# Kernel tuning notes

Measured on AMD Instinct MI355X. Metric: run time of the kernel, lower is better.

Reference implementation:

```python
import jax, jax.numpy as jnp
import numpy as np

N = 100000
E = 1600000
F_IN = 128
HID = 64
HEADS = 2
OUT_HEADS = 1
NUM_CLASS = 18
NEG_SLOPE = 0.2


def setup_inputs() -> dict:
    key = jax.random.key(0)
    ks = jax.random.split(key, 12)
    x = jax.random.normal(ks[0], (N, F_IN), dtype=jnp.float32)
    edge_index = jax.random.randint(ks[1], (2, E), 0, N, dtype=jnp.int64)
    s = lambda k, shp, fan: jax.random.normal(k, shp, dtype=jnp.float32) * (1.0 / np.sqrt(fan))
    W0 = s(ks[2], (F_IN, HID), F_IN)
    b0 = jnp.zeros((HID,), dtype=jnp.float32)
    W1 = s(ks[3], (HID, HEADS * HID), HID)
    att_src1 = s(ks[4], (HEADS, HID), HID)
    att_dst1 = s(ks[5], (HEADS, HID), HID)
    b1 = jnp.zeros((HEADS * HID,), dtype=jnp.float32)
    W2 = s(ks[6], (HEADS * HID, OUT_HEADS * NUM_CLASS), HEADS * HID)
    att_src2 = s(ks[7], (OUT_HEADS, NUM_CLASS), NUM_CLASS)
    att_dst2 = s(ks[8], (OUT_HEADS, NUM_CLASS), NUM_CLASS)
    b2 = jnp.zeros((OUT_HEADS * NUM_CLASS,), dtype=jnp.float32)
    return {"x": x, "edge_index": edge_index, "W0": W0, "b0": b0,
            "W1": W1, "att_src1": att_src1, "att_dst1": att_dst1, "b1": b1,
            "W2": W2, "att_src2": att_src2, "att_dst2": att_dst2, "b2": b2}


def gat_conv(x, src, dst, W, att_s, att_d, bias, heads, out_ch):
    n = x.shape[0]
    h = (x @ W).reshape(n, heads, out_ch)              # [N,H,C]
    a_s = jnp.sum(h * att_s, axis=-1)                   # [N,H]
    a_d = jnp.sum(h * att_d, axis=-1)                   # [N,H]
    e = jax.nn.leaky_relu(a_s[src] + a_d[dst], NEG_SLOPE)  # [E,H]
    m = jax.ops.segment_max(e, dst, num_segments=n)
    ex = jnp.exp(e - m[dst])
    denom = jax.ops.segment_sum(ex, dst, num_segments=n)
    alpha = ex / denom[dst]                              # [E,H]
    msg = h[src] * alpha[:, :, None]                     # [E,H,C]
    out = jax.ops.segment_sum(msg, dst, num_segments=n)  # [N,H,C]
    return out.reshape(n, heads * out_ch) + bias


def reference(x, edge_index, W0, b0, W1, att_src1, att_dst1, b1, W2, att_src2, att_dst2, b2):
    n = x.shape[0]
    # PyG GATConv adds self-loops by default
    loops = jnp.arange(n, dtype=edge_index.dtype)
    src = jnp.concatenate([edge_index[0], loops])
    dst = jnp.concatenate([edge_index[1], loops])
    # eval mode: dropout is identity
    h = jax.nn.relu(x @ W0 + b0)
    h = jax.nn.elu(gat_conv(h, src, dst, W1, att_src1, att_dst1, b1, HEADS, HID))
    out = gat_conv(h, src, dst, W2, att_src2, att_dst2, b2, OUT_HEADS, NUM_CLASS)
    return jax.nn.log_softmax(out, axis=-1)
```

## Files before the change

### kernel.cpp

```cpp
#include <hip/hip_runtime.h>
#include <math.h>


#define NEG_SLOPE 0.2f
#define STASH_CAP 128

typedef unsigned short ushort_t;

__device__ __forceinline__ float wmax(float v) {
    for (int o = 32; o; o >>= 1) v = fmaxf(v, __shfl_xor(v, o));
    return v;
}
__device__ __forceinline__ float wsum(float v) {
    for (int o = 32; o; o >>= 1) v += __shfl_xor(v, o);
    return v;
}

__device__ __forceinline__ unsigned bfpack(float a, float b) {
    unsigned ua = __float_as_uint(a);
    unsigned ub = __float_as_uint(b);
    ua = (ua + 0x7fffu + ((ua >> 16) & 1u)) >> 16;
    ub = (ub + 0x7fffu + ((ub >> 16) & 1u)) & 0xffff0000u;
    return ua | ub;
}
__device__ __forceinline__ ushort_t bf16of(float a) {
    unsigned ua = __float_as_uint(a);
    return (ushort_t)((ua + 0x7fffu + ((ua >> 16) & 1u)) >> 16);
}
__device__ __forceinline__ float bflo(unsigned u) { return __uint_as_float(u << 16); }
__device__ __forceinline__ float bfhi(unsigned u) { return __uint_as_float(u & 0xffff0000u); }
__device__ __forceinline__ float bfval(ushort_t u) { return __uint_as_float(((unsigned)u) << 16); }

__global__ void k_deg_init(int* __restrict__ deg, int N) {
    int i = blockIdx.x * blockDim.x + threadIdx.x;
    if (i < N) deg[i] = 1;
}
__global__ void k_deg_edges(const int* __restrict__ ei, int* __restrict__ deg,
                            int* __restrict__ eofs, int E) {
    int e = blockIdx.x * blockDim.x + threadIdx.x;
    if (e < E) eofs[e] = atomicAdd(&deg[ei[E + e]], 1);
}

__global__ __launch_bounds__(256) void k_scan1(const int* __restrict__ deg, int* __restrict__ rs,
                                               int* __restrict__ bsum, int N) {
    __shared__ int s[256];
    int t = threadIdx.x;
    int base = blockIdx.x * 1024;
    int i0 = base + t * 4;
    int d0 = (i0 + 0 < N) ? deg[i0 + 0] : 0;
    int d1 = (i0 + 1 < N) ? deg[i0 + 1] : 0;
    int d2 = (i0 + 2 < N) ? deg[i0 + 2] : 0;
    int d3 = (i0 + 3 < N) ? deg[i0 + 3] : 0;
    int s0 = d0, s1 = s0 + d1, s2 = s1 + d2, s3 = s2 + d3;
    int tsum = s3;
    s[t] = tsum;
    __syncthreads();
    for (int off = 1; off < 256; off <<= 1) {
        int v = (t >= off) ? s[t - off] : 0;
        __syncthreads();
        s[t] += v;
        __syncthreads();
    }
    int excl = s[t] - tsum;
    if (i0 + 0 < N) rs[1 + i0 + 0] = excl + s0;
    if (i0 + 1 < N) rs[1 + i0 + 1] = excl + s1;
    if (i0 + 2 < N) rs[1 + i0 + 2] = excl + s2;
    if (i0 + 3 < N) rs[1 + i0 + 3] = excl + s3;
    if (t == 0) bsum[blockIdx.x] = s[255];
}

__global__ __launch_bounds__(256) void k_scan2(const int* __restrict__ bsum,
                                               int* __restrict__ boff, int NB) {
    __shared__ int s[256];
    int t = threadIdx.x;
    int orig = (t < NB) ? bsum[t] : 0;
    s[t] = orig;
    __syncthreads();
    for (int off = 1; off < 256; off <<= 1) {
        int v = (t >= off) ? s[t - off] : 0;
        __syncthreads();
        s[t] += v;
        __syncthreads();
    }
    if (t < NB) boff[t] = s[t] - orig;
}

__global__ void k_scan3(int* __restrict__ rs, const int* __restrict__ boff, int N) {
    int i = blockIdx.x * blockDim.x + threadIdx.x;
    if (i == 0) rs[0] = 0;
    if (i < N) rs[1 + i] += boff[i >> 10];
}

__global__ __launch_bounds__(256) void k_scatter(const int* __restrict__ ei,
                                                 const int* __restrict__ eofs,
                                                 const int* __restrict__ rs,
                                                 int* __restrict__ csr,
                                                 int E, int Etot, int cohortBlocks) {
    int c = blockIdx.x & 7;
    int pb = blockIdx.x >> 3;
    int tid = pb * 256 + threadIdx.x;
    int stride = cohortBlocks * 256;
    for (int e = tid; e < Etot; e += stride) {
        int dst = (e < E) ? ei[E + e] : (e - E);
        if (((dst >> 13) & 7) != c) continue;
        int src, ofs;
        if (e < E) { src = ei[e]; ofs = eofs[e]; } else { src = dst; ofs = 0; }
        csr[rs[dst] + ofs] = src;
    }
}


__global__ __launch_bounds__(256) void k_gemm1(const float* __restrict__ x,
                                               const float* __restrict__ W0,
                                               const float* __restrict__ b0,
                                               unsigned* __restrict__ h0b, int N) {
    __shared__ float wl[128 * 64];
    __shared__ float al[64 * 132];
    int t = threadIdx.x;
    int n0 = blockIdx.x * 64;
    const float4* wg = (const float4*)W0;
    float4* wl4 = (float4*)wl;
#pragma unroll
    for (int i = 0; i < 8; ++i) wl4[t + i * 256] = wg[t + i * 256];
#pragma unroll
    for (int i = 0; i < 8; ++i) {
        int f = t + i * 256;
        int node = f >> 5, q = f & 31;
        int ng = n0 + node; if (ng > N - 1) ng = N - 1;
        float4 v = ((const float4*)x)[(size_t)ng * 32 + q];
        *(float4*)&al[node * 132 + q * 4] = v;
    }
    __syncthreads();
    int colg = t & 15;
    int rowg = t >> 4;
    float4 acc[4];
#pragma unroll
    for (int j = 0; j < 4; ++j) acc[j] = make_float4(0.f, 0.f, 0.f, 0.f);
    for (int k4 = 0; k4 < 128; k4 += 4) {
        float4 w0 = *(float4*)&wl[(k4 + 0) * 64 + colg * 4];
        float4 w1 = *(float4*)&wl[(k4 + 1) * 64 + colg * 4];
        float4 w2 = *(float4*)&wl[(k4 + 2) * 64 + colg * 4];
        float4 w3 = *(float4*)&wl[(k4 + 3) * 64 + colg * 4];
#pragma unroll
        for (int j = 0; j < 4; ++j) {
            float4 a = *(float4*)&al[(rowg * 4 + j) * 132 + k4];
            acc[j].x += a.x * w0.x + a.y * w1.x + a.z * w2.x + a.w * w3.x;
            acc[j].y += a.x * w0.y + a.y * w1.y + a.z * w2.y + a.w * w3.y;
            acc[j].z += a.x * w0.z + a.y * w1.z + a.z * w2.z + a.w * w3.z;
            acc[j].w += a.x * w0.w + a.y * w1.w + a.z * w2.w + a.w * w3.w;
        }
    }
    float4 bb = ((const float4*)b0)[colg];
#pragma unroll
    for (int j = 0; j < 4; ++j) {
        int n = n0 + rowg * 4 + j;
        if (n < N) {
            float rx = fmaxf(acc[j].x + bb.x, 0.f);
            float ry = fmaxf(acc[j].y + bb.y, 0.f);
            float rz = fmaxf(acc[j].z + bb.z, 0.f);
            float rw = fmaxf(acc[j].w + bb.w, 0.f);
            uint2 pr; pr.x = bfpack(rx, ry); pr.y = bfpack(rz, rw);
            ((uint2*)h0b)[(size_t)n * 16 + colg] = pr;
        }
    }
}

__global__ __launch_bounds__(256) void k_gemm2(const unsigned* __restrict__ h0b,
                                               const float* __restrict__ W1,
                                               const float* __restrict__ as_g,
                                               const float* __restrict__ ad_g,
                                               ushort_t* __restrict__ h1b,
                                               float* __restrict__ as1,
                                               float* __restrict__ ad1, int N) {
    __shared__ float wl[64 * 128];
    __shared__ float al[64 * 68];
    int t = threadIdx.x;
    int n0 = blockIdx.x * 64;
    const float4* wg = (const float4*)W1;
    float4* wl4 = (float4*)wl;
#pragma unroll
    for (int i = 0; i < 8; ++i) wl4[t + i * 256] = wg[t + i * 256];
#pragma unroll
    for (int i = 0; i < 2; ++i) {
        int f = t + i * 256;
        int node = f >> 3, q = f & 7;
        int ng = n0 + node; if (ng > N - 1) ng = N - 1;
        uint4 u = ((const uint4*)h0b)[(size_t)ng * 8 + q];
        float* dst = &al[node * 68 + q * 8];
        dst[0] = bflo(u.x); dst[1] = bfhi(u.x);
        dst[2] = bflo(u.y); dst[3] = bfhi(u.y);
        dst[4] = bflo(u.z); dst[5] = bfhi(u.z);
        dst[6] = bflo(u.w); dst[7] = bfhi(u.w);
    }
    __syncthreads();
    int colg = t & 31;
    int rowg = t >> 5;
    float4 acc[8];
#pragma unroll
    for (int j = 0; j < 8; ++j) acc[j] = make_float4(0.f, 0.f, 0.f, 0.f);
    for (int k4 = 0; k4 < 64; k4 += 4) {
        float4 w0 = *(float4*)&wl[(k4 + 0) * 128 + colg * 4];
        float4 w1 = *(float4*)&wl[(k4 + 1) * 128 + colg * 4];
        float4 w2 = *(float4*)&wl[(k4 + 2) * 128 + colg * 4];
        float4 w3 = *(float4*)&wl[(k4 + 3) * 128 + colg * 4];
#pragma unroll
        for (int j = 0; j < 8; ++j) {
            float4 a = *(float4*)&al[(rowg * 8 + j) * 68 + k4];
            acc[j].x += a.x * w0.x + a.y * w1.x + a.z * w2.x + a.w * w3.x;
            acc[j].y += a.x * w0.y + a.y * w1.y + a.z * w2.y + a.w * w3.y;
            acc[j].z += a.x * w0.z + a.y * w1.z + a.z * w2.z + a.w * w3.z;
            acc[j].w += a.x * w0.w + a.y * w1.w + a.z * w2.w + a.w * w3.w;
        }
    }
    float4 asv = ((const float4*)as_g)[colg];
    float4 adv = ((const float4*)ad_g)[colg];
    float ps[8], pd[8];
#pragma unroll
    for (int j = 0; j < 8; ++j) {
        ps[j] = acc[j].x * asv.x + acc[j].y * asv.y + acc[j].z * asv.z + acc[j].w * asv.w;
        pd[j] = acc[j].x * adv.x + acc[j].y * adv.y + acc[j].z * adv.z + acc[j].w * adv.w;
    }
    for (int o = 1; o < 16; o <<= 1) {
#pragma unroll
        for (int j = 0; j < 8; ++j) {
            ps[j] += __shfl_xor(ps[j], o);
            pd[j] += __shfl_xor(pd[j], o);
        }
    }
#pragma unroll
    for (int j = 0; j < 8; ++j) {
        int n = n0 + rowg * 8 + j;
        if (n < N) {
            uint2 pr;
            pr.x = bfpack(acc[j].x, acc[j].y);
            pr.y = bfpack(acc[j].z, acc[j].w);
            ((uint2*)h1b)[(size_t)n * 32 + colg] = pr;
        }
    }
    int lane = t & 63;
    if ((lane & 15) == 0) {
        int head = (lane >> 4) & 1;
#pragma unroll
        for (int j = 0; j < 8; ++j) {
            int n = n0 + rowg * 8 + j;
            if (n < N) {
                as1[n * 2 + head] = ps[j];
                ad1[n * 2 + head] = pd[j];
            }
        }
    }
}

__global__ __launch_bounds__(256) void k_node_l1(const int* __restrict__ rs,
                                                 const int* __restrict__ csr,
                                                 const ushort_t* __restrict__ h1b,
                                                 const float* __restrict__ as1,
                                                 const float* __restrict__ ad1,
                                                 const float* __restrict__ b1,
                                                 unsigned* __restrict__ aggb, int N) {
    __shared__ float2 stashA[4][128];
    __shared__ float4 stashE[4][STASH_CAP];
    int wid = threadIdx.x >> 6;
    int lane = threadIdx.x & 63;
    int n = (blockIdx.x * 256 + threadIdx.x) >> 6;
    if (n >= N) return;
    int row = rs[n], end = rs[n + 1];
    int deg = end - row;
    float2 adv = ((const float2*)ad1)[n];
    const float2* asp = (const float2*)as1;
    const char* h1base = (const char*)h1b;
    int eg = lane >> 4;
    int fl = lane & 15;
    int head_off = (fl >= 8) ? 64 : 0;
    int flbase = fl * 16;
    float acc[8] = {0.f, 0.f, 0.f, 0.f, 0.f, 0.f, 0.f, 0.f};
    float inv0, inv1;
    if (deg <= 64) {
        bool act = lane < deg;
        int src = act ? csr[row + lane] : 0;
        float2 av = asp[src];
        float e0 = av.x + adv.x, e1 = av.y + adv.y;
        e0 = e0 > 0.f ? e0 : NEG_SLOPE * e0;
        e1 = e1 > 0.f ? e1 : NEG_SLOPE * e1;
        if (!act) { e0 = -INFINITY; e1 = -INFINITY; }
        float m0 = wmax(e0), m1 = wmax(e1);
        float p0 = act ? __expf(e0 - m0) : 0.f;
        float p1 = act ? __expf(e1 - m1) : 0.f;
        inv0 = __builtin_amdgcn_rcpf(wsum(p0));
        inv1 = __builtin_amdgcn_rcpf(wsum(p1));
        stashA[wid][lane] = make_float2(__int_as_float(src), p0);
        stashA[wid][64 + lane] = make_float2(__int_as_float(src), p1);
        for (int j = 0; j < deg; j += 4) {
            float2 sa = stashA[wid][head_off + j + eg];
            int sj = __float_as_int(sa.x);
            float aj = sa.y;
            uint4 u = *(const uint4*)(h1base + (((unsigned)sj) << 8) + flbase);
            acc[0] += bflo(u.x) * aj; acc[1] += bfhi(u.x) * aj;
            acc[2] += bflo(u.y) * aj; acc[3] += bfhi(u.y) * aj;
            acc[4] += bflo(u.z) * aj; acc[5] += bfhi(u.z) * aj;
            acc[6] += bflo(u.w) * aj; acc[7] += bfhi(u.w) * aj;
        }
    } else {
        inv0 = 1.f; inv1 = 1.f;
        float m0 = -INFINITY, m1 = -INFINITY, l0 = 0.f, l1 = 0.f;
        for (int base = row; base < end; base += 64) {
            int idx = base + lane;
            bool act = idx < end;
            int src = act ? csr[idx] : 0;
            float2 av = asp[src];
            float e0 = av.x + adv.x, e1 = av.y + adv.y;
            e0 = e0 > 0.f ? e0 : NEG_SLOPE * e0;
            e1 = e1 > 0.f ? e1 : NEG_SLOPE * e1;
            int sidx = idx - row;
            if (act && sidx < STASH_CAP)
                stashE[wid][sidx] = make_float4(__int_as_float(src), e0, e1, 0.f);
            if (!act) { e0 = -INFINITY; e1 = -INFINITY; }
            float m0n = fmaxf(m0, wmax(e0));
            float m1n = fmaxf(m1, wmax(e1));
            float p0 = act ? __expf(e0 - m0n) : 0.f;
            float p1 = act ? __expf(e1 - m1n) : 0.f;
            l0 = l0 * __expf(m0 - m0n) + wsum(p0);
            l1 = l1 * __expf(m1 - m1n) + wsum(p1);
            m0 = m0n; m1 = m1n;
        }
        float r0 = __builtin_amdgcn_rcpf(l0);
        float r1 = __builtin_amdgcn_rcpf(l1);
        for (int base = row; base < end; base += 64) {
            int idx = base + lane;
            bool act = idx < end;
            int sidx = idx - row;
            int src; float e0, e1;
            if (sidx < STASH_CAP) {
                float4 se = stashE[wid][sidx];
                src = __float_as_int(se.x);
                e0 = se.y; e1 = se.z;
            } else {
                src = act ? csr[idx] : 0;
                float2 av = asp[src];
                e0 = av.x + adv.x; e1 = av.y + adv.y;
                e0 = e0 > 0.f ? e0 : NEG_SLOPE * e0;
                e1 = e1 > 0.f ? e1 : NEG_SLOPE * e1;
            }
            if (!act) src = 0;
            float a0 = act ? __expf(e0 - m0) * r0 : 0.f;
            float a1 = act ? __expf(e1 - m1) * r1 : 0.f;
            stashA[wid][lane] = make_float2(__int_as_float(src), a0);
            stashA[wid][64 + lane] = make_float2(__int_as_float(src), a1);
            int cnt = min(64, end - base);
            for (int j = 0; j < cnt; j += 4) {
                float2 sa = stashA[wid][head_off + j + eg];
                int sj = __float_as_int(sa.x);
                float aj = sa.y;
                uint4 u = *(const uint4*)(h1base + (((unsigned)sj) << 8) + flbase);
                acc[0] += bflo(u.x) * aj; acc[1] += bfhi(u.x) * aj;
                acc[2] += bflo(u.y) * aj; acc[3] += bfhi(u.y) * aj;
                acc[4] += bflo(u.z) * aj; acc[5] += bfhi(u.z) * aj;
                acc[6] += bflo(u.w) * aj; acc[7] += bfhi(u.w) * aj;
            }
        }
    }
#pragma unroll
    for (int i = 0; i < 8; ++i) {
        acc[i] += __shfl_xor(acc[i], 16);
        acc[i] += __shfl_xor(acc[i], 32);
    }
    if (lane < 16) {
        float inv = (lane >= 8) ? inv1 : inv0;
        float4 ba = ((const float4*)b1)[lane * 2];
        float4 bb4 = ((const float4*)b1)[lane * 2 + 1];
        float v[8];
        v[0] = acc[0] * inv + ba.x;  v[1] = acc[1] * inv + ba.y;
        v[2] = acc[2] * inv + ba.z;  v[3] = acc[3] * inv + ba.w;
        v[4] = acc[4] * inv + bb4.x; v[5] = acc[5] * inv + bb4.y;
        v[6] = acc[6] * inv + bb4.z; v[7] = acc[7] * inv + bb4.w;
#pragma unroll
        for (int i = 0; i < 8; ++i) v[i] = v[i] > 0.f ? v[i] : __expf(v[i]) - 1.f;
        uint4 pk;
        pk.x = bfpack(v[0], v[1]); pk.y = bfpack(v[2], v[3]);
        pk.z = bfpack(v[4], v[5]); pk.w = bfpack(v[6], v[7]);
        ((uint4*)aggb)[(size_t)n * 16 + lane] = pk;
    }
}

__global__ __launch_bounds__(256, 4) void k_node2(const unsigned* __restrict__ aggb,
                                                  const float* __restrict__ W2,
                                                  const float* __restrict__ as_g,
                                                  const float* __restrict__ ad_g,
                                                  ushort_t* __restrict__ h2b,
                                                  float* __restrict__ a_s,
                                                  float* __restrict__ a_d, int N) {
    __shared__ float al[64 * 132];
    __shared__ float w2t[20 * 132];
    int t = threadIdx.x;
    int n0 = blockIdx.x * 64;
#pragma unroll
    for (int i = 0; i < 4; ++i) {
        int f = t + i * 256;
        int node = f >> 4, q = f & 15;
        int ng = n0 + node; if (ng > N - 1) ng = N - 1;
        uint4 u = ((const uint4*)aggb)[(size_t)ng * 16 + q];
        float* dst = &al[node * 132 + q * 8];
        dst[0] = bflo(u.x); dst[1] = bfhi(u.x);
        dst[2] = bflo(u.y); dst[3] = bfhi(u.y);
        dst[4] = bflo(u.z); dst[5] = bfhi(u.z);
        dst[6] = bflo(u.w); dst[7] = bfhi(u.w);
    }
    for (int i = t; i < 2560; i += 256) {
        int c = i >> 7, k = i & 127;
        w2t[c * 132 + k] = (c < 18) ? W2[k * 18 + c] : 0.f;
    }
    __syncthreads();
    int node = t >> 2;
    int cq = t & 3;
    int c0 = cq * 5;
    int n = n0 + node;
    float acc[5] = {0.f, 0.f, 0.f, 0.f, 0.f};
#pragma unroll 2
    for (int k4 = 0; k4 < 128; k4 += 4) {
        float4 a = *(float4*)&al[node * 132 + k4];
#pragma unroll
        for (int i = 0; i < 5; ++i) {
            float4 w = *(float4*)&w2t[(c0 + i) * 132 + k4];
            acc[i] += a.x * w.x + a.y * w.y + a.z * w.z + a.w * w.w;
        }
    }
    float ps = 0.f, pd = 0.f;
#pragma unroll
    for (int i = 0; i < 5; ++i) {
        int c = c0 + i;
        float asv = (c < 18) ? as_g[c] : 0.f;
        float adv = (c < 18) ? ad_g[c] : 0.f;
        ps += acc[i] * asv;
        pd += acc[i] * adv;
    }
    ps += __shfl_xor(ps, 1); ps += __shfl_xor(ps, 2);
    pd += __shfl_xor(pd, 1); pd += __shfl_xor(pd, 2);
    if (n < N) {
#pragma unroll
        for (int i = 0; i < 5; ++i) {
            int c = c0 + i;
            if (c < 18) h2b[(size_t)n * 24 + c] = bf16of(acc[i]);
        }
        if (cq == 0) { a_s[n] = ps; a_d[n] = pd; }
    }
}

__global__ __launch_bounds__(256) void k_node_l2(const int* __restrict__ rs,
                                                 const int* __restrict__ csr,
                                                 const ushort_t* __restrict__ h2b,
                                                 const float* __restrict__ as2,
                                                 const float* __restrict__ ad2,
                                                 const float* __restrict__ b2,
                                                 float* __restrict__ out, int N) {
    __shared__ float2 stash[4][STASH_CAP];
    int wid = threadIdx.x >> 6;
    int lane = threadIdx.x & 63;
    int n = (blockIdx.x * 256 + threadIdx.x) >> 6;
    if (n >= N) return;
    int row = rs[n], end = rs[n + 1];
    int deg = end - row;
    float adn = ad2[n];
    int g = lane / 21;
    int c = lane - g * 21;
    int cc = c < 18 ? c : 17;
    float acc = 0.f;
    float post;
    if (deg <= 64) {
        bool act = lane < deg;
        int src = act ? csr[row + lane] : 0;
        float e = as2[src] + adn;
        e = e > 0.f ? e : NEG_SLOPE * e;
        if (!act) e = -INFINITY;
        float m = wmax(e);
        float p = act ? __expf(e - m) : 0.f;
        post = __builtin_amdgcn_rcpf(wsum(p));
        stash[wid][lane] = make_float2(__int_as_float(src), p);
        for (int o = g; o < deg; o += 3) {
            float2 se = stash[wid][o];
            int src2 = __float_as_int(se.x);
            acc += se.y * bfval(h2b[(size_t)src2 * 24 + cc]);
        }
    } else {
        post = 1.f;
        float m = -INFINITY, l = 0.f;
        for (int base = row; base < end; base += 64) {
            int idx = base + lane;
            bool act = idx < end;
            int src = act ? csr[idx] : 0;
            float e = as2[src] + adn;
            e = e > 0.f ? e : NEG_SLOPE * e;
            int sidx = idx - row;
            if (act && sidx < STASH_CAP)
                stash[wid][sidx] = make_float2(__int_as_float(src), e);
            if (!act) e = -INFINITY;
            float mn = fmaxf(m, wmax(e));
            float p = act ? __expf(e - mn) : 0.f;
            l = l * __expf(m - mn) + wsum(p);
            m = mn;
        }
        float invl = __builtin_amdgcn_rcpf(l);
        int lim = deg < STASH_CAP ? deg : STASH_CAP;
        for (int o = g; o < lim; o += 3) {
            float2 se = stash[wid][o];
            int src = __float_as_int(se.x);
            float alpha = __expf(se.y - m) * invl;
            acc += alpha * bfval(h2b[(size_t)src * 24 + cc]);
        }
        for (int pos = row + STASH_CAP + g; pos < end; pos += 3) {
            int src = csr[pos];
            float e = as2[src] + adn;
            e = e > 0.f ? e : NEG_SLOPE * e;
            float alpha = __expf(e - m) * invl;
            acc += alpha * bfval(h2b[(size_t)src * 24 + cc]);
        }
    }
    float t1 = __shfl(acc, (lane + 21) & 63);
    float t2 = __shfl(acc, (lane + 42) & 63);
    acc += t1 + t2;
    float bb = (lane < 18) ? b2[lane] : 0.f;
    float v = acc * post + bb;
    float tmx = (lane < 18) ? v : -INFINITY;
    for (int o = 16; o; o >>= 1) tmx = fmaxf(tmx, __shfl_xor(tmx, o));
    float s = (lane < 18) ? __expf(v - tmx) : 0.f;
    for (int o = 16; o; o >>= 1) s += __shfl_xor(s, o);
    float lse = tmx + __logf(s);
    if (lane < 18) out[(size_t)n * 18 + lane] = v - lse;
}

extern "C" void kernel_launch(void* const* d_in, const int* in_sizes, int n_in,
                              void* d_out, int out_size, void* d_ws, size_t ws_size,
                              hipStream_t stream) {
    const float* x      = (const float*)d_in[0];
    const int*   ei     = (const int*)d_in[1];
    const float* W0     = (const float*)d_in[2];
    const float* b0     = (const float*)d_in[3];
    const float* W1     = (const float*)d_in[4];
    const float* att_s1 = (const float*)d_in[5];
    const float* att_d1 = (const float*)d_in[6];
    const float* b1     = (const float*)d_in[7];
    const float* W2     = (const float*)d_in[8];
    const float* att_s2 = (const float*)d_in[9];
    const float* att_d2 = (const float*)d_in[10];
    const float* b2     = (const float*)d_in[11];

    const int N = in_sizes[0] / 128;
    const int E = in_sizes[1] / 2;
    const int Etot = E + N;
    const int NB = (N + 1023) / 1024;
    const int NBLK = (N + 63) / 64;

    char* w = (char*)d_ws;
    unsigned* h0b  = (unsigned*)w; w += (size_t)N * 64 * 2;
    ushort_t* h1b  = (ushort_t*)w; w += (size_t)N * 128 * 2;
    unsigned* aggb = (unsigned*)w; w += (size_t)N * 128 * 2;
    float* as1     = (float*)w;    w += (size_t)N * 2 * 4;
    float* ad1     = (float*)w;    w += (size_t)N * 2 * 4;
    ushort_t* h2b  = (ushort_t*)w; w += (size_t)N * 24 * 2;
    float* as2     = (float*)w;    w += (size_t)N * 4;
    float* ad2     = (float*)w;    w += (size_t)N * 4;
    int* deg       = (int*)w;      w += (size_t)N * 4;
    int* rs        = (int*)w;      w += (size_t)(N + 1) * 4;
    int* bsum      = (int*)w;      w += (size_t)256 * 4;
    int* boff      = (int*)w;      w += (size_t)256 * 4;
    int* eofs      = (int*)w;      w += (size_t)E * 4;
    int* csr       = (int*)w;      w += (size_t)Etot * 4;

    float* out = (float*)d_out;

    k_deg_init<<<(N + 255) / 256, 256, 0, stream>>>(deg, N);
    k_deg_edges<<<(E + 255) / 256, 256, 0, stream>>>(ei, deg, eofs, E);
    k_scan1<<<NB, 256, 0, stream>>>(deg, rs, bsum, N);
    k_scan2<<<1, 256, 0, stream>>>(bsum, boff, NB);
    k_scan3<<<(N + 255) / 256, 256, 0, stream>>>(rs, boff, N);
    const int cohortBlocks = 128;
    k_scatter<<<8 * cohortBlocks, 256, 0, stream>>>(ei, eofs, rs, csr, E, Etot, cohortBlocks);

    k_gemm1<<<NBLK, 256, 0, stream>>>(x, W0, b0, h0b, N);
    k_gemm2<<<NBLK, 256, 0, stream>>>(h0b, W1, att_s1, att_d1, h1b, as1, ad1, N);

    k_node_l1<<<(N * 64 + 255) / 256, 256, 0, stream>>>(rs, csr, h1b, as1, ad1, b1, aggb, N);

    k_node2<<<NBLK, 256, 0, stream>>>(aggb, W2, att_s2, att_d2, h2b, as2, ad2, N);
    k_node_l2<<<(N * 64 + 255) / 256, 256, 0, stream>>>(rs, csr, h2b, as2, ad2, b2, out, N);
}
```

Measured before the change: 446.8 us.

## Simplify high-degree paths, pad LDS stash, use raw bf16 high-half, memset degrees

Several small changes land together. The degree-init kernel becomes hipMemsetAsync, with the +1 for self-loops folded into the scan and into the scatter offset. The shared-memory edge stash for high-degree nodes is removed in both aggregation kernels, which now recompute edge scores from csr. The per-head LDS stash is padded from offset 64 to 68, presumably to cut bank conflicts. The high bf16 half is read without masking off the low 16 bits, which saves an AND per element but leaves those bits in as noise in the low mantissa.

Measured after the change: 451.1 us. About the same (+1.0%).

```diff
diff --git a/kernel.cpp b/kernel.cpp
--- a/kernel.cpp
+++ b/kernel.cpp
@@ -3,7 +3,6 @@
 
 
 #define NEG_SLOPE 0.2f
-#define STASH_CAP 128
 
 typedef unsigned short ushort_t;
 
@@ -29,12 +28,9 @@
 }
 __device__ __forceinline__ float bflo(unsigned u) { return __uint_as_float(u << 16); }
 __device__ __forceinline__ float bfhi(unsigned u) { return __uint_as_float(u & 0xffff0000u); }
+__device__ __forceinline__ float bfhiraw(unsigned u) { return __uint_as_float(u); }
 __device__ __forceinline__ float bfval(ushort_t u) { return __uint_as_float(((unsigned)u) << 16); }
 
-__global__ void k_deg_init(int* __restrict__ deg, int N) {
-    int i = blockIdx.x * blockDim.x + threadIdx.x;
-    if (i < N) deg[i] = 1;
-}
 __global__ void k_deg_edges(const int* __restrict__ ei, int* __restrict__ deg,
                             int* __restrict__ eofs, int E) {
     int e = blockIdx.x * blockDim.x + threadIdx.x;
@@ -47,10 +43,10 @@
     int t = threadIdx.x;
     int base = blockIdx.x * 1024;
     int i0 = base + t * 4;
-    int d0 = (i0 + 0 < N) ? deg[i0 + 0] : 0;
-    int d1 = (i0 + 1 < N) ? deg[i0 + 1] : 0;
-    int d2 = (i0 + 2 < N) ? deg[i0 + 2] : 0;
-    int d3 = (i0 + 3 < N) ? deg[i0 + 3] : 0;
+    int d0 = (i0 + 0 < N) ? deg[i0 + 0] + 1 : 0;
+    int d1 = (i0 + 1 < N) ? deg[i0 + 1] + 1 : 0;
+    int d2 = (i0 + 2 < N) ? deg[i0 + 2] + 1 : 0;
+    int d3 = (i0 + 3 < N) ? deg[i0 + 3] + 1 : 0;
     int s0 = d0, s1 = s0 + d1, s2 = s1 + d2, s3 = s2 + d3;
     int tsum = s3;
     s[t] = tsum;
@@ -104,7 +100,7 @@
         int dst = (e < E) ? ei[E + e] : (e - E);
         if (((dst >> 13) & 7) != c) continue;
         int src, ofs;
-        if (e < E) { src = ei[e]; ofs = eofs[e]; } else { src = dst; ofs = 0; }
+        if (e < E) { src = ei[e]; ofs = 1 + eofs[e]; } else { src = dst; ofs = 0; }
         csr[rs[dst] + ofs] = src;
     }
 }
@@ -258,8 +254,7 @@
                                                  const float* __restrict__ ad1,
                                                  const float* __restrict__ b1,
                                                  unsigned* __restrict__ aggb, int N) {
-    __shared__ float2 stashA[4][128];
-    __shared__ float4 stashE[4][STASH_CAP];
+    __shared__ float2 stashA[4][136];
     int wid = threadIdx.x >> 6;
     int lane = threadIdx.x & 63;
     int n = (blockIdx.x * 256 + threadIdx.x) >> 6;
@@ -271,7 +266,7 @@
     const char* h1base = (const char*)h1b;
     int eg = lane >> 4;
     int fl = lane & 15;
-    int head_off = (fl >= 8) ? 64 : 0;
+    int head_off = (fl >= 8) ? 68 : 0;
     int flbase = fl * 16;
     float acc[8] = {0.f, 0.f, 0.f, 0.f, 0.f, 0.f, 0.f, 0.f};
     float inv0, inv1;
@@ -289,16 +284,16 @@
         inv0 = __builtin_amdgcn_rcpf(wsum(p0));
         inv1 = __builtin_amdgcn_rcpf(wsum(p1));
         stashA[wid][lane] = make_float2(__int_as_float(src), p0);
-        stashA[wid][64 + lane] = make_float2(__int_as_float(src), p1);
+        stashA[wid][68 + lane] = make_float2(__int_as_float(src), p1);
         for (int j = 0; j < deg; j += 4) {
             float2 sa = stashA[wid][head_off + j + eg];
             int sj = __float_as_int(sa.x);
             float aj = sa.y;
             uint4 u = *(const uint4*)(h1base + (((unsigned)sj) << 8) + flbase);
-            acc[0] += bflo(u.x) * aj; acc[1] += bfhi(u.x) * aj;
-            acc[2] += bflo(u.y) * aj; acc[3] += bfhi(u.y) * aj;
-            acc[4] += bflo(u.z) * aj; acc[5] += bfhi(u.z) * aj;
-            acc[6] += bflo(u.w) * aj; acc[7] += bfhi(u.w) * aj;
+            acc[0] += bflo(u.x) * aj; acc[1] += bfhiraw(u.x) * aj;
+            acc[2] += bflo(u.y) * aj; acc[3] += bfhiraw(u.y) * aj;
+            acc[4] += bflo(u.z) * aj; acc[5] += bfhiraw(u.z) * aj;
+            acc[6] += bflo(u.w) * aj; acc[7] += bfhiraw(u.w) * aj;
         }
     } else {
         inv0 = 1.f; inv1 = 1.f;
@@ -311,9 +306,6 @@
             float e0 = av.x + adv.x, e1 = av.y + adv.y;
             e0 = e0 > 0.f ? e0 : NEG_SLOPE * e0;
             e1 = e1 > 0.f ? e1 : NEG_SLOPE * e1;
-            int sidx = idx - row;
-            if (act && sidx < STASH_CAP)
-                stashE[wid][sidx] = make_float4(__int_as_float(src), e0, e1, 0.f);
             if (!act) { e0 = -INFINITY; e1 = -INFINITY; }
             float m0n = fmaxf(m0, wmax(e0));
             float m1n = fmaxf(m1, wmax(e1));
@@ -328,34 +320,25 @@
         for (int base = row; base < end; base += 64) {
             int idx = base + lane;
             bool act = idx < end;
-            int sidx = idx - row;
-            int src; float e0, e1;
-            if (sidx < STASH_CAP) {
-                float4 se = stashE[wid][sidx];
-                src = __float_as_int(se.x);
-                e0 = se.y; e1 = se.z;
-            } else {
-                src = act ? csr[idx] : 0;
-                float2 av = asp[src];
-                e0 = av.x + adv.x; e1 = av.y + adv.y;
-                e0 = e0 > 0.f ? e0 : NEG_SLOPE * e0;
-                e1 = e1 > 0.f ? e1 : NEG_SLOPE * e1;
-            }
-            if (!act) src = 0;
+            int src = act ? csr[idx] : 0;
+            float2 av = asp[src];
+            float e0 = av.x + adv.x, e1 = av.y + adv.y;
+            e0 = e0 > 0.f ? e0 : NEG_SLOPE * e0;
+            e1 = e1 > 0.f ? e1 : NEG_SLOPE * e1;
             float a0 = act ? __expf(e0 - m0) * r0 : 0.f;
             float a1 = act ? __expf(e1 - m1) * r1 : 0.f;
             stashA[wid][lane] = make_float2(__int_as_float(src), a0);
-            stashA[wid][64 + lane] = make_float2(__int_as_float(src), a1);
+            stashA[wid][68 + lane] = make_float2(__int_as_float(src), a1);
             int cnt = min(64, end - base);
             for (int j = 0; j < cnt; j += 4) {
                 float2 sa = stashA[wid][head_off + j + eg];
                 int sj = __float_as_int(sa.x);
                 float aj = sa.y;
                 uint4 u = *(const uint4*)(h1base + (((unsigned)sj) << 8) + flbase);
-                acc[0] += bflo(u.x) * aj; acc[1] += bfhi(u.x) * aj;
-                acc[2] += bflo(u.y) * aj; acc[3] += bfhi(u.y) * aj;
-                acc[4] += bflo(u.z) * aj; acc[5] += bfhi(u.z) * aj;
-                acc[6] += bflo(u.w) * aj; acc[7] += bfhi(u.w) * aj;
+                acc[0] += bflo(u.x) * aj; acc[1] += bfhiraw(u.x) * aj;
+                acc[2] += bflo(u.y) * aj; acc[3] += bfhiraw(u.y) * aj;
+                acc[4] += bflo(u.z) * aj; acc[5] += bfhiraw(u.z) * aj;
+                acc[6] += bflo(u.w) * aj; acc[7] += bfhiraw(u.w) * aj;
             }
         }
     }
@@ -452,7 +435,7 @@
                                                  const float* __restrict__ ad2,
                                                  const float* __restrict__ b2,
                                                  float* __restrict__ out, int N) {
-    __shared__ float2 stash[4][STASH_CAP];
+    __shared__ float2 stash[4][64];
     int wid = threadIdx.x >> 6;
     int lane = threadIdx.x & 63;
     int n = (blockIdx.x * 256 + threadIdx.x) >> 6;
@@ -489,9 +472,6 @@
             int src = act ? csr[idx] : 0;
             float e = as2[src] + adn;
             e = e > 0.f ? e : NEG_SLOPE * e;
-            int sidx = idx - row;
-            if (act && sidx < STASH_CAP)
-                stash[wid][sidx] = make_float2(__int_as_float(src), e);
             if (!act) e = -INFINITY;
             float mn = fmaxf(m, wmax(e));
             float p = act ? __expf(e - mn) : 0.f;
@@ -499,14 +479,7 @@
             m = mn;
         }
         float invl = __builtin_amdgcn_rcpf(l);
-        int lim = deg < STASH_CAP ? deg : STASH_CAP;
-        for (int o = g; o < lim; o += 3) {
-            float2 se = stash[wid][o];
-            int src = __float_as_int(se.x);
-            float alpha = __expf(se.y - m) * invl;
-            acc += alpha * bfval(h2b[(size_t)src * 24 + cc]);
-        }
-        for (int pos = row + STASH_CAP + g; pos < end; pos += 3) {
+        for (int pos = row + g; pos < end; pos += 3) {
             int src = csr[pos];
             float e = as2[src] + adn;
             e = e > 0.f ? e : NEG_SLOPE * e;
@@ -567,7 +540,7 @@
 
     float* out = (float*)d_out;
 
-    k_deg_init<<<(N + 255) / 256, 256, 0, stream>>>(deg, N);
+    hipMemsetAsync(deg, 0, (size_t)N * 4, stream);
     k_deg_edges<<<(E + 255) / 256, 256, 0, stream>>>(ei, deg, eofs, E);
     k_scan1<<<NB, 256, 0, stream>>>(deg, rs, bsum, N);
     k_scan2<<<1, 256, 0, stream>>>(bsum, boff, NB);
```
